# Optimization experiments

Hardware: AMD Instinct MI355X
Metric: run time of the kernel (lower is better)

## Reference

```python
import jax, jax.numpy as jnp
import numpy as np

N, M, D = 100000, 50000, 256
NE = N + M
B = 131072

def kl_normal_std(mu, scale):
    # KL( N(mu, scale) || N(0, 1) ) = -log(scale) + (scale^2 + mu^2)/2 - 1/2
    return 0.5 * (scale * scale + mu * mu - 1.0) - jnp.log(scale)

def setup_inputs() -> dict:
    key = jax.random.key(0)
    ks = jax.random.split(key, 8)
    users = jax.random.randint(ks[0], (B, 1), 0, N)
    items = jax.random.randint(ks[1], (B, 1), N, NE)
    x = jnp.concatenate([users, items], axis=1)                        # [B, 2]
    bias_table = jax.random.normal(ks[2], (NE, 2), dtype=jnp.float32)
    entity_table = jax.random.normal(ks[3], (NE, 2 * D), dtype=jnp.float32)
    global_bias_mean = jnp.zeros((1,), dtype=jnp.float32)
    global_bias_scale = jnp.ones((1,), dtype=jnp.float32)
    nb_occ = jax.random.randint(ks[4], (NE,), 1, 1001)                 # train occurrence counts >= 1
    eps_bias = jax.random.normal(ks[5], (NE,), dtype=jnp.float32)
    eps_entity = jax.random.normal(ks[6], (NE, D), dtype=jnp.float32)
    eps_global = jax.random.normal(ks[7], (1,), dtype=jnp.float32)
    return {"x": x, "bias_table": bias_table, "entity_table": entity_table,
            "global_bias_mean": global_bias_mean, "global_bias_scale": global_bias_scale,
            "nb_occ": nb_occ, "eps_bias": eps_bias, "eps_entity": eps_entity,
            "eps_global": eps_global}

def reference(x, bias_table, entity_table, global_bias_mean, global_bias_scale,
              nb_occ, eps_bias, eps_entity, eps_global):
    # --- reparameterized samples (one eps per table row == one eps per unique entity) ---
    gb_scale = jnp.abs(global_bias_scale)
    global_bias = global_bias_mean + gb_scale * eps_global             # [1]

    bias_mu = bias_table[:, 0]
    bias_sc = jnp.abs(bias_table[:, 1])
    biases_all = bias_mu + bias_sc * eps_bias                          # [NE]

    ent_mu = entity_table[:, :D]
    ent_sc = jnp.abs(entity_table[:, D:])
    entities_all = ent_mu + ent_sc * eps_entity                        # [NE, D]

    # --- FM forward: bias sum + product-sum interaction ---
    pair_bias = biases_all[x].sum(axis=1)                              # [B]
    pair_emb = (entities_all[x[:, 0]] * entities_all[x[:, 1]]).sum(axis=1)  # [B]
    logits = global_bias + pair_bias + pair_emb                        # [B] (Bernoulli logits)

    # --- closed-form KL vs N(0,1), rescaled by batch/train occupancy ---
    kl_bias = kl_normal_std(bias_mu, bias_sc)                          # [NE]
    kl_entity = kl_normal_std(ent_mu, ent_sc).sum(axis=1)              # [NE]

    nb_occ_f = nb_occ.astype(jnp.float32)
    cnt = jnp.bincount(x.reshape(-1), length=NE).astype(jnp.float32)   # nb_occ_in_batch
    cnt_u = jnp.bincount(x[:, 0], length=NE).astype(jnp.float32)
    cnt_i = jnp.bincount(x[:, 1], length=NE).astype(jnp.float32)
    user_norm = (cnt_u / nb_occ_f).sum()
    item_norm = (cnt_i / nb_occ_f).sum()

    ids = jnp.arange(NE)
    scale_term = (jnp.where(ids <= N, float(N), 0.0) / user_norm
                  + jnp.where(ids > N, float(M), 0.0) / item_norm)
    kl_rescaled = ((kl_bias + kl_entity) * (cnt / nb_occ_f) * scale_term).sum()

    kl_global = kl_normal_std(global_bias_mean, gb_scale).sum()
    return logits, kl_global + kl_rescaled
```

## Files before the change

### kernel.cpp

```cpp
#include <hip/hip_runtime.h>
#include <math.h>

#define NU   100000
#define MI   50000
#define NEn  150000
#define Bp   131072

typedef float    f4v __attribute__((ext_vector_type(4)));
typedef _Float16 h8v __attribute__((ext_vector_type(8)));
typedef _Float16 h4v __attribute__((ext_vector_type(4)));

__device__ __forceinline__ float wred(float v) {
#pragma unroll
    for (int m = 32; m > 0; m >>= 1) v += __shfl_xor(v, m, 64);
    return v;
}
__device__ __forceinline__ float hred(float v) {
#pragma unroll
    for (int m = 16; m > 0; m >>= 1) v += __shfl_xor(v, m, 64);
    return v;
}

__global__ __launch_bounds__(256) void k_ent(
    const f4v* __restrict__ et,
    const f4v* __restrict__ epse,
    const float* __restrict__ bt,
    const float* __restrict__ epsb,
    const float* __restrict__ gbm,
    const float* __restrict__ gbs,
    h4v*   __restrict__ enth,
    float* __restrict__ bia,
    float* __restrict__ klpe,
    float* __restrict__ hdr,
    float* __restrict__ outkl)
{
    if (blockIdx.x == 0) {
        if (threadIdx.x < 128) hdr[threadIdx.x] = 0.f;
        if (threadIdx.x == 0) {
            float gm = gbm[0], gs = fabsf(gbs[0]);
            outkl[0] = 0.5f * (gs * gs + gm * gm - 1.0f) - __logf(gs);
        }
    }

    int lane = threadIdx.x & 63;
    int e    = blockIdx.x * 4 + (threadIdx.x >> 6);

    const f4v* row = et + (size_t)e * 128;
    f4v mu = __builtin_nontemporal_load(row + lane);
    f4v s4 = __builtin_nontemporal_load(row + 64 + lane);
    f4v ep = __builtin_nontemporal_load(epse + (size_t)e * 64 + lane);
    float scx = fabsf(s4.x), scy = fabsf(s4.y), scz = fabsf(s4.z), scw = fabsf(s4.w);

    if (enth) {
        h4v oh;
        oh.x = (_Float16)fmaf(scx, ep.x, mu.x);
        oh.y = (_Float16)fmaf(scy, ep.y, mu.y);
        oh.z = (_Float16)fmaf(scz, ep.z, mu.z);
        oh.w = (_Float16)fmaf(scw, ep.w, mu.w);
        enth[(size_t)e * 64 + lane] = oh;
    }

    float kl = 0.5f * (scx * scx + mu.x * mu.x - 1.0f) - __logf(scx)
             + 0.5f * (scy * scy + mu.y * mu.y - 1.0f) - __logf(scy)
             + 0.5f * (scz * scz + mu.z * mu.z - 1.0f) - __logf(scz)
             + 0.5f * (scw * scw + mu.w * mu.w - 1.0f) - __logf(scw);
    kl = wred(kl);

    if (lane == 0) {
        float bmu = bt[2 * e];
        float bsc = fabsf(bt[2 * e + 1]);
        bia[e]  = fmaf(bsc, epsb[e], bmu);
        klpe[e] = kl + 0.5f * (bsc * bsc + bmu * bmu - 1.0f) - __logf(bsc);
    }
}

__global__ __launch_bounds__(256) void k_log(
    const int2* __restrict__ x2,
    const h8v* __restrict__ enth,
    const float* __restrict__ bia,
    const float* __restrict__ klpe,
    const int* __restrict__ nb,
    const float* __restrict__ gbm, const float* __restrict__ gbs,
    const float* __restrict__ epsg,
    float* __restrict__ hdr,
    float* __restrict__ out)
{
    const int lane = threadIdx.x & 63;
    const int sub  = lane & 31;
    const int p    = blockIdx.x * 8 + ((threadIdx.x >> 6) << 1) + (lane >> 5);
    const bool use_ent = (enth != nullptr);

    int2 pr = x2[p];
    int u = pr.x, v = pr.y;

    if (use_ent) {
        float bu = bia[u];
        float bv = bia[v];
        h8v a = enth[(size_t)u * 32 + sub];
        h8v b = enth[(size_t)v * 32 + sub];
        float d = 0.f;
#pragma unroll
        for (int i = 0; i < 8; ++i) d = fmaf((float)a[i], (float)b[i], d);
        d = hred(d);
        if (sub == 0) {
            float gb = fmaf(fabsf(gbs[0]), epsg[0], gbm[0]);
            __builtin_nontemporal_store(gb + bu + bv + d, out + p);
        }
    }

    float uS = 0.f, iS = 0.f, aS = 0.f, bS = 0.f;
    if (sub == 0) {
        float rnu = 1.0f / (float)nb[u];
        float rnv = 1.0f / (float)nb[v];
        float au  = klpe[u] * rnu;
        float av  = klpe[v] * rnv;
        uS = rnu;
        iS = rnv;
        aS = au + ((v == NU) ? av : 0.f);
        bS = ((v > NU) ? av : 0.f);
    }
    uS = wred(uS); iS = wred(iS); aS = wred(aS); bS = wred(bS);

    __shared__ float s[4][4];
    int wib = threadIdx.x >> 6;
    if (lane == 0) { s[wib][0] = uS; s[wib][1] = iS; s[wib][2] = aS; s[wib][3] = bS; }
    __syncthreads();
    if (threadIdx.x < 4) {
        float t = s[0][threadIdx.x] + s[1][threadIdx.x]
                + s[2][threadIdx.x] + s[3][threadIdx.x];
        atomicAdd(hdr + (blockIdx.x & 31) * 4 + threadIdx.x, t);
    }
}

__global__ void k_fin(const float* __restrict__ hdr, float* __restrict__ outkl) {
    if (threadIdx.x == 0) {
        float U = 0.f, I = 0.f, A = 0.f, Bv = 0.f;
#pragma unroll
        for (int i = 0; i < 32; ++i) {
            U  += hdr[i * 4 + 0];
            I  += hdr[i * 4 + 1];
            A  += hdr[i * 4 + 2];
            Bv += hdr[i * 4 + 3];
        }
        outkl[0] += (float)NU * A / U + (float)MI * Bv / I;
    }
}

__global__ __launch_bounds__(256) void k_logits_rc(
    const int* __restrict__ x, const float4* __restrict__ et,
    const float4* __restrict__ epse, const float* __restrict__ bia,
    const float* __restrict__ gbm, const float* __restrict__ gbs,
    const float* __restrict__ epsg, float* __restrict__ out)
{
    int lane = threadIdx.x & 63;
    int p    = blockIdx.x * 4 + (threadIdx.x >> 6);
    int u = x[2 * p], v = x[2 * p + 1];
    const float4* ru = et + (size_t)u * 128;
    const float4* rv = et + (size_t)v * 128;
    float4 mu_u = ru[lane], s_u = ru[64 + lane], e_u = epse[(size_t)u * 64 + lane];
    float4 mu_v = rv[lane], s_v = rv[64 + lane], e_v = epse[(size_t)v * 64 + lane];
    float ax = fmaf(fabsf(s_u.x), e_u.x, mu_u.x), bx = fmaf(fabsf(s_v.x), e_v.x, mu_v.x);
    float ay = fmaf(fabsf(s_u.y), e_u.y, mu_u.y), by = fmaf(fabsf(s_v.y), e_v.y, mu_v.y);
    float az = fmaf(fabsf(s_u.z), e_u.z, mu_u.z), bz = fmaf(fabsf(s_v.z), e_v.z, mu_v.z);
    float aw = fmaf(fabsf(s_u.w), e_u.w, mu_u.w), bw = fmaf(fabsf(s_v.w), e_v.w, mu_v.w);
    float d = ax * bx + ay * by + az * bz + aw * bw;
    d = wred(d);
    if (lane == 0) {
        float gb = fmaf(fabsf(gbs[0]), epsg[0], gbm[0]);
        out[p] = gb + bia[u] + bia[v] + d;
    }
}

extern "C" void kernel_launch(void* const* d_in, const int* in_sizes, int n_in,
                              void* d_out, int out_size, void* d_ws, size_t ws_size,
                              hipStream_t stream)
{
    const int*   x    = (const int*)d_in[0];
    const float* bt   = (const float*)d_in[1];
    const float* et   = (const float*)d_in[2];
    const float* gbm  = (const float*)d_in[3];
    const float* gbs  = (const float*)d_in[4];
    const int*   nb   = (const int*)d_in[5];
    const float* epsb = (const float*)d_in[6];
    const float* epse = (const float*)d_in[7];
    const float* epsg = (const float*)d_in[8];
    float* out = (float*)d_out;

    char*  ws   = (char*)d_ws;
    float* hdr  = (float*)ws;
    float* klpe = (float*)(ws + 512);
    float* bia  = (float*)(ws + 512 + (size_t)NEn * 4);
    size_t entoff = 512 + (size_t)NEn * 8;
    h4v* enth = nullptr;
    if (ws_size >= entoff + (size_t)NEn * 512)
        enth = (h4v*)(ws + entoff);


    k_ent<<<NEn / 4, 256, 0, stream>>>(
        (const f4v*)et, (const f4v*)epse, bt, epsb,
        gbm, gbs, enth, bia, klpe, hdr, out + Bp);

    k_log<<<Bp / 8, 256, 0, stream>>>(
        (const int2*)x, (const h8v*)enth, bia, klpe, nb,
        gbm, gbs, epsg, hdr, out);

    if (!enth)
        k_logits_rc<<<Bp / 4, 256, 0, stream>>>(x, (const float4*)et,
                                                (const float4*)epse, bia,
                                                gbm, gbs, epsg, out);

    k_fin<<<1, 64, 0, stream>>>(hdr, out + Bp);
}
```

Measured before the change: 550.3 us.

## Split KL reduction into dedicated dense blocks separate from logits blocks

The combined logits/KL kernel is split by block index. The first 512 blocks handle the KL reduction with one pair per thread, so every lane does useful work and no lanes sit idle. The remaining blocks compute logits only, at two pairs per wave. Atomic slots drop from 32 to 8 and the number of atomics is much smaller, at the cost of more contention on each slot.

After: 519.9 us, median of 2. 1.06x faster.

```diff
diff --git a/kernel.cpp b/kernel.cpp
--- a/kernel.cpp
+++ b/kernel.cpp
@@ -5,6 +5,9 @@
 #define MI   50000
 #define NEn  150000
 #define Bp   131072
+
+#define PB   512
+#define NSLOT 8
 
 typedef float    f4v __attribute__((ext_vector_type(4)));
 typedef _Float16 h8v __attribute__((ext_vector_type(8)));
@@ -35,7 +38,7 @@
     float* __restrict__ outkl)
 {
     if (blockIdx.x == 0) {
-        if (threadIdx.x < 128) hdr[threadIdx.x] = 0.f;
+        if (threadIdx.x < 4 * NSLOT) hdr[threadIdx.x] = 0.f;
         if (threadIdx.x == 0) {
             float gm = gbm[0], gs = fabsf(gbs[0]);
             outkl[0] = 0.5f * (gs * gs + gm * gm - 1.0f) - __logf(gs);
@@ -85,50 +88,50 @@
     float* __restrict__ hdr,
     float* __restrict__ out)
 {
-    const int lane = threadIdx.x & 63;
-    const int sub  = lane & 31;
-    const int p    = blockIdx.x * 8 + ((threadIdx.x >> 6) << 1) + (lane >> 5);
-    const bool use_ent = (enth != nullptr);
-
-    int2 pr = x2[p];
-    int u = pr.x, v = pr.y;
-
-    if (use_ent) {
-        float bu = bia[u];
-        float bv = bia[v];
-        h8v a = enth[(size_t)u * 32 + sub];
-        h8v b = enth[(size_t)v * 32 + sub];
-        float d = 0.f;
-#pragma unroll
-        for (int i = 0; i < 8; ++i) d = fmaf((float)a[i], (float)b[i], d);
-        d = hred(d);
-        if (sub == 0) {
-            float gb = fmaf(fabsf(gbs[0]), epsg[0], gbm[0]);
-            __builtin_nontemporal_store(gb + bu + bv + d, out + p);
-        }
-    }
-
-    float uS = 0.f, iS = 0.f, aS = 0.f, bS = 0.f;
-    if (sub == 0) {
+    if (blockIdx.x < PB) {
+        int p = blockIdx.x * 256 + threadIdx.x;
+        int2 pr = x2[p];
+        int u = pr.x, v = pr.y;
         float rnu = 1.0f / (float)nb[u];
         float rnv = 1.0f / (float)nb[v];
         float au  = klpe[u] * rnu;
         float av  = klpe[v] * rnv;
-        uS = rnu;
-        iS = rnv;
-        aS = au + ((v == NU) ? av : 0.f);
-        bS = ((v > NU) ? av : 0.f);
-    }
-    uS = wred(uS); iS = wred(iS); aS = wred(aS); bS = wred(bS);
-
-    __shared__ float s[4][4];
-    int wib = threadIdx.x >> 6;
-    if (lane == 0) { s[wib][0] = uS; s[wib][1] = iS; s[wib][2] = aS; s[wib][3] = bS; }
-    __syncthreads();
-    if (threadIdx.x < 4) {
-        float t = s[0][threadIdx.x] + s[1][threadIdx.x]
-                + s[2][threadIdx.x] + s[3][threadIdx.x];
-        atomicAdd(hdr + (blockIdx.x & 31) * 4 + threadIdx.x, t);
+        float uS = rnu;
+        float iS = rnv;
+        float aS = au + ((v == NU) ? av : 0.f);
+        float bS = ((v > NU) ? av : 0.f);
+
+        uS = wred(uS); iS = wred(iS); aS = wred(aS); bS = wred(bS);
+        __shared__ float s[4][4];
+        int wib = threadIdx.x >> 6;
+        if ((threadIdx.x & 63) == 0) {
+            s[wib][0] = uS; s[wib][1] = iS; s[wib][2] = aS; s[wib][3] = bS;
+        }
+        __syncthreads();
+        if (threadIdx.x < 4) {
+            float t = s[0][threadIdx.x] + s[1][threadIdx.x]
+                    + s[2][threadIdx.x] + s[3][threadIdx.x];
+            atomicAdd(hdr + (blockIdx.x & (NSLOT - 1)) * 4 + threadIdx.x, t);
+        }
+        return;
+    }
+
+    int lane = threadIdx.x & 63;
+    int sub  = lane & 31;
+    int p    = (blockIdx.x - PB) * 8 + ((threadIdx.x >> 6) << 1) + (lane >> 5);
+    int2 pr = x2[p];
+    int u = pr.x, v = pr.y;
+    float bu = bia[u];
+    float bv = bia[v];
+    h8v a = enth[(size_t)u * 32 + sub];
+    h8v b = enth[(size_t)v * 32 + sub];
+    float d = 0.f;
+#pragma unroll
+    for (int i = 0; i < 8; ++i) d = fmaf((float)a[i], (float)b[i], d);
+    d = hred(d);
+    if (sub == 0) {
+        float gb = fmaf(fabsf(gbs[0]), epsg[0], gbm[0]);
+        __builtin_nontemporal_store(gb + bu + bv + d, out + p);
     }
 }
 
@@ -136,7 +139,7 @@
     if (threadIdx.x == 0) {
         float U = 0.f, I = 0.f, A = 0.f, Bv = 0.f;
 #pragma unroll
-        for (int i = 0; i < 32; ++i) {
+        for (int i = 0; i < NSLOT; ++i) {
             U  += hdr[i * 4 + 0];
             I  += hdr[i * 4 + 1];
             A  += hdr[i * 4 + 2];
@@ -200,14 +203,18 @@
         (const f4v*)et, (const f4v*)epse, bt, epsb,
         gbm, gbs, enth, bia, klpe, hdr, out + Bp);
 
-    k_log<<<Bp / 8, 256, 0, stream>>>(
-        (const int2*)x, (const h8v*)enth, bia, klpe, nb,
-        gbm, gbs, epsg, hdr, out);
-
-    if (!enth)
+    if (enth) {
+        k_log<<<PB + Bp / 8, 256, 0, stream>>>(
+            (const int2*)x, (const h8v*)enth, bia, klpe, nb,
+            gbm, gbs, epsg, hdr, out);
+    } else {
+        k_log<<<PB, 256, 0, stream>>>(
+            (const int2*)x, nullptr, bia, klpe, nb,
+            gbm, gbs, epsg, hdr, out);
         k_logits_rc<<<Bp / 4, 256, 0, stream>>>(x, (const float4*)et,
                                                 (const float4*)epse, bia,
                                                 gbm, gbs, epsg, out);
+    }
 
     k_fin<<<1, 64, 0, stream>>>(hdr, out + Bp);
 }
```
